# Kernel tuning notes

Measured on AMD Instinct MI355X. Metric: run time of the kernel, lower is better.

Reference implementation:

```python
import jax, jax.numpy as jnp
import numpy as np

CONF_THRESH = 0.25
IOU_THRESH = 0.45
MAX_PER_IMG = 100
K_PRE = 512          # fixed pre-NMS candidate count (padding for jit)
CLS_OFFSET = 4096.0  # class offset for non-class-agnostic NMS (torchvision batched_nms trick)


def setup_inputs() -> dict:
    key = jax.random.key(0)
    k1, k2, k3, k4 = jax.random.split(key, 4)
    B, N, C = 32, 8400, 80
    # YOLOX raw output layout: (cx, cy, w, h, obj, cls_0..cls_C-1)
    cxcy = jax.random.uniform(k1, (B, N, 2), dtype=jnp.float32) * 640.0
    wh = jax.random.uniform(k2, (B, N, 2), dtype=jnp.float32) * 128.0 + 4.0
    obj = jax.random.uniform(k3, (B, N, 1), dtype=jnp.float32)
    cls = jax.random.uniform(k4, (B, N, C), dtype=jnp.float32)
    pred = jnp.concatenate([cxcy, wh, obj, cls], axis=-1)  # [B, N, 85]
    return {"pred": pred}


def _pairwise_iou(b):
    # b: [K, 4] xyxy -> [K, K] IoU
    x1 = jnp.maximum(b[:, None, 0], b[None, :, 0])
    y1 = jnp.maximum(b[:, None, 1], b[None, :, 1])
    x2 = jnp.minimum(b[:, None, 2], b[None, :, 2])
    y2 = jnp.minimum(b[:, None, 3], b[None, :, 3])
    inter = jnp.clip(x2 - x1, 0.0) * jnp.clip(y2 - y1, 0.0)
    area = (b[:, 2] - b[:, 0]) * (b[:, 3] - b[:, 1])
    union = area[:, None] + area[None, :] - inter
    return inter / (union + 1e-9)


def _nms(boxes, valid):
    # boxes [K,4] already sorted by score desc; valid [K] bool. Greedy NMS.
    iou = _pairwise_iou(boxes)

    def body(i, keep):
        # keep[j] is False for j >= i, so this only checks earlier kept boxes
        suppressed = jnp.any(keep & (iou[i] > IOU_THRESH))
        return keep.at[i].set(valid[i] & jnp.logical_not(suppressed))

    return jax.lax.fori_loop(0, K_PRE, body, jnp.zeros(K_PRE, dtype=bool))


def reference(pred):
    # --- box decode: cxcywh -> xyxy (YOLOX postprocess box_corner) ---
    half = pred[..., 2:4] * 0.5
    boxes = jnp.concatenate([pred[..., :2] - half, pred[..., :2] + half], axis=-1)  # [B,N,4]
    obj = pred[..., 4]                 # [B,N]
    cls = pred[..., 5:]                # [B,N,C]
    class_conf = cls.max(axis=-1)      # [B,N]
    class_pred = jnp.argmax(cls, axis=-1)  # [B,N] int
    scores = obj * class_conf          # [B,N]

    # per-image adaptive conf: min(conf_thresh, best score) -> at least 1 survives
    conf = jnp.minimum(CONF_THRESH, scores.max(axis=-1, keepdims=True))  # [B,1]
    valid = scores >= conf
    masked = jnp.where(valid, scores, -jnp.inf)

    # fixed-size candidate set, sorted by score desc
    top_scores, idx = jax.lax.top_k(masked, K_PRE)  # [B,K]
    b_k = jnp.take_along_axis(boxes, idx[..., None], axis=1)       # [B,K,4]
    obj_k = jnp.take_along_axis(obj, idx, axis=1)                  # [B,K]
    cc_k = jnp.take_along_axis(class_conf, idx, axis=1)            # [B,K]
    cp_k = jnp.take_along_axis(class_pred, idx, axis=1)            # [B,K]
    valid_k = jnp.isfinite(top_scores)

    # class_agnostic=False: offset boxes by class so cross-class IoU is 0
    nms_boxes = b_k + cp_k.astype(b_k.dtype)[..., None] * CLS_OFFSET
    keep = jax.vmap(_nms)(nms_boxes, valid_k)  # [B,K] bool

    # compact kept boxes to the front (stable argsort preserves score order)
    order = jnp.argsort(jnp.where(keep, jnp.arange(K_PRE), K_PRE), axis=-1)
    sel = order[:, :MAX_PER_IMG]                                   # [B,M]
    mask = jnp.take_along_axis(keep, sel, axis=1)                  # [B,M]

    dets = jnp.concatenate(
        [b_k, obj_k[..., None], cc_k[..., None], cp_k.astype(b_k.dtype)[..., None]],
        axis=-1,
    )  # [B,K,7] = (x1,y1,x2,y2,obj,class_conf,class_pred)
    dets = jnp.take_along_axis(dets, sel[..., None], axis=1)       # [B,M,7]
    dets = dets * mask[..., None].astype(dets.dtype)
    return dets, mask
```

## Files before the change

### kernel.cpp

```cpp
#include <hip/hip_runtime.h>

#define NB 32
#define NN 8400
#define NC 80
#define KPRE 512
#define MAXOUT 100
#define NGRP 263
#define NWV 526

__global__ __launch_bounds__(128) void score_kernel(const float* __restrict__ pred,
                                                    float* __restrict__ scores,
                                                    unsigned* __restrict__ wmaxg,
                                                    float4* __restrict__ rawbox,
                                                    float4* __restrict__ minfo) {
    int b = blockIdx.y;
    int w = threadIdx.x >> 6, lane = threadIdx.x & 63;
    int g = blockIdx.x * 2 + w;
    __shared__ float4 stg4[2][340];
    const float4* p4 = (const float4*)pred;
    size_t base4 = (size_t)b * 178500 + (size_t)g * 340;
    size_t img_end4 = ((size_t)b + 1) * 178500;
    for (int k = lane; k < 340; k += 64) {
        size_t e = base4 + k;
        if (e >= img_end4) e = img_end4 - 1;
        stg4[w][k] = p4[e];
    }
    int rl = lane >> 2, q = lane & 3;
    int row = g * 16 + rl;
    const float* r = (const float*)&stg4[w][0] + rl * 85;
    float cx = r[0], cy = r[1], bw = r[2], bh = r[3], obj = r[4];
    int c0 = 5 + q * 20;
    float cc = r[c0];
    int cp = q * 20;
    for (int c = 1; c < 20; c++) {
        float v = r[c0 + c];
        if (v > cc) { cc = v; cp = q * 20 + c; }
    }
    {
        float cc1 = __shfl_xor(cc, 1, 64); int cp1 = __shfl_xor(cp, 1, 64);
        bool take = (cc1 > cc) || (cc1 == cc && cp1 < cp);
        cc = take ? cc1 : cc; cp = take ? cp1 : cp;
        float cc2 = __shfl_xor(cc, 2, 64); int cp2 = __shfl_xor(cp, 2, 64);
        take = (cc2 > cc) || (cc2 == cc && cp2 < cp);
        cc = take ? cc2 : cc; cp = take ? cp2 : cp;
    }
    float s = __fmul_rn(obj, cc);
    float hw = __fmul_rn(bw, 0.5f), hh = __fmul_rn(bh, 0.5f);
    float x1 = cx - hw, y1 = cy - hh, x2 = cx + hw, y2 = cy + hh;
    int srcl = (lane & 15) * 4;
    float v0 = __shfl(x1, srcl, 64);
    float v1 = __shfl(y1, srcl, 64);
    float v2 = __shfl(x2, srcl, 64);
    float v3 = __shfl(y2, srcl, 64);
    float v4 = __shfl(obj, srcl, 64);
    float v5 = __shfl(cc, srcl, 64);
    int   v6 = __shfl(cp, srcl, 64);
    float v7 = __shfl(s, srcl, 64);
    int wrow = g * 16 + (lane & 15);
    if (lane < 16 && wrow < NN) {
        size_t idx = (size_t)b * NN + wrow;
        scores[idx] = v7;
        rawbox[idx] = make_float4(v0, v1, v2, v3);
        minfo[idx]  = make_float4(v4, v5, (float)v6, v7);
    }
    if (row >= NN) s = 0.0f;
    unsigned bits = __float_as_uint(s);
    for (int o = 32; o > 0; o >>= 1) {
        unsigned other = (unsigned)__shfl_down((int)bits, o, 64);
        if (other > bits) bits = other;
    }
    if (lane == 0) wmaxg[b * NWV + g] = bits;
}

__device__ __forceinline__ void find_bin(const unsigned* hist, int cstart, unsigned T, int lane,
                                         int* outB, unsigned* outR) {
    unsigned running = 0;
    unsigned v = hist[cstart * 64 + lane];
    for (int c = cstart; c >= 0; c--) {
        unsigned vn = (c > 0) ? hist[(c - 1) * 64 + lane] : 0u;
        unsigned s = v;
        for (int off = 1; off < 64; off <<= 1) {
            unsigned u = (unsigned)__shfl_down((int)s, off, 64);
            if (lane + off < 64) s += u;
        }
        unsigned total0 = (unsigned)__shfl((int)s, 0, 64);
        if (total0 + running >= T) {
            unsigned long long mask = __ballot(s + running >= T);
            int m = 63 - __clzll(mask);
            unsigned sm = (unsigned)__shfl((int)s, m, 64);
            unsigned vm = (unsigned)__shfl((int)v, m, 64);
            if (lane == 0) { *outB = c * 64 + m; *outR = T - (sm + running - vm); }
            return;
        }
        running += total0;
        v = vn;
    }
    if (lane == 0) { *outB = 0; *outR = T; }
}

__device__ __forceinline__ void find_bin4(const uint4* h4, int cstart, unsigned T, int lane,
                                          int* outB, unsigned* outR) {
    unsigned running = 0;
    uint4 q = h4[cstart * 64 + lane];
    for (int c = cstart; c >= 0; c--) {
        uint4 qn;
        if (c > 0) qn = h4[(c - 1) * 64 + lane];
        else { qn.x = 0; qn.y = 0; qn.z = 0; qn.w = 0; }
        unsigned v = q.x + q.y + q.z + q.w;
        unsigned s = v;
        for (int off = 1; off < 64; off <<= 1) {
            unsigned u = (unsigned)__shfl_down((int)s, off, 64);
            if (lane + off < 64) s += u;
        }
        unsigned total0 = (unsigned)__shfl((int)s, 0, 64);
        if (total0 + running >= T) {
            unsigned long long mask = __ballot(s + running >= T);
            int m = 63 - __clzll(mask);
            unsigned sm = (unsigned)__shfl((int)s, m, 64);
            unsigned vm = (unsigned)__shfl((int)v, m, 64);
            if (lane == 0) { *outB = c * 64 + m; *outR = T - (sm + running - vm); }
            return;
        }
        running += total0;
        q = qn;
    }
    if (lane == 0) { *outB = 0; *outR = T; }
}

__global__ __launch_bounds__(1024) void selnms_kernel(const float* __restrict__ scores,
                                                      const unsigned* __restrict__ wmaxg,
                                                      const float4* __restrict__ rawbox,
                                                      const float4* __restrict__ minfo,
                                                      float* __restrict__ out) {
    int b = blockIdx.x, t = threadIdx.x;
    int lane = t & 63;
    __shared__ unsigned histB[2048];
    __shared__ unsigned long long list[KPRE];
    __shared__ unsigned long long sorted[KPRE];
    __shared__ unsigned long long elist64[256];
    __shared__ float4 sb[KPRE];
    __shared__ float4 sraw[KPRE];
    __shared__ float4 smeta[KPRE];
    __shared__ float  sarea[KPRE];
    __shared__ unsigned long long siou[KPRE * 8];
    __shared__ unsigned long long skeep[8];
    __shared__ int S_B[2];
    __shared__ unsigned S_T[2];
    __shared__ int S_cnt, S_ecnt, S_done;
    __shared__ float S_conf;
    __shared__ unsigned S_mbits;

    unsigned* histA4 = (unsigned*)siou;
    int hcopy = (t >> 8) & 3;

    if (t == 0) { S_cnt = 0; S_ecnt = 0; S_done = 0; }
    if (t < 64) {
        unsigned tmp[9];
#pragma unroll
        for (int k = 0; k < 9; k++) {
            int i = t + k * 64;
            tmp[k] = (i < NWV) ? wmaxg[b * NWV + i] : 0u;
        }
        unsigned m = 0;
#pragma unroll
        for (int k = 0; k < 9; k++) if (tmp[k] > m) m = tmp[k];
        for (int off = 32; off > 0; off >>= 1) {
            unsigned o = (unsigned)__shfl_down((int)m, off, 64);
            if (o > m) m = o;
        }
        if (t == 0) { S_conf = fminf(0.25f, __uint_as_float(m)); S_mbits = m; }
    }
    for (int i = t; i < 8192; i += 1024) histA4[i] = 0;
    for (int i = t; i < 2048; i += 1024) histB[i] = 0;
    if (t < 256) elist64[t] = 0ull;
    __syncthreads();
    float conf = S_conf;
    const float4* sc4 = (const float4*)(scores + (size_t)b * NN);
    unsigned ka[8];
    unsigned kb[4] = {0u, 0u, 0u, 0u};
    {
        float4 u0 = sc4[2 * t], u1 = sc4[2 * t + 1];
        ka[0] = (u0.x >= conf) ? __float_as_uint(u0.x) : 0u;
        ka[1] = (u0.y >= conf) ? __float_as_uint(u0.y) : 0u;
        ka[2] = (u0.z >= conf) ? __float_as_uint(u0.z) : 0u;
        ka[3] = (u0.w >= conf) ? __float_as_uint(u0.w) : 0u;
        ka[4] = (u1.x >= conf) ? __float_as_uint(u1.x) : 0u;
        ka[5] = (u1.y >= conf) ? __float_as_uint(u1.y) : 0u;
        ka[6] = (u1.z >= conf) ? __float_as_uint(u1.z) : 0u;
        ka[7] = (u1.w >= conf) ? __float_as_uint(u1.w) : 0u;
        if (t < 52) {
            float4 u2 = sc4[2048 + t];
            kb[0] = (u2.x >= conf) ? __float_as_uint(u2.x) : 0u;
            kb[1] = (u2.y >= conf) ? __float_as_uint(u2.y) : 0u;
            kb[2] = (u2.z >= conf) ? __float_as_uint(u2.z) : 0u;
            kb[3] = (u2.w >= conf) ? __float_as_uint(u2.w) : 0u;
        }
#pragma unroll
        for (int j = 0; j < 8; j++) {
            unsigned k = ka[j];
            if (k) atomicAdd(&histA4[((k >> 21) << 2) | hcopy], 1u);
        }
        if (t < 52) {
#pragma unroll
            for (int j = 0; j < 4; j++) {
                unsigned k = kb[j];
                if (k) atomicAdd(&histA4[((k >> 21) << 2) | hcopy], 1u);
            }
        }
    }
    __syncthreads();
    if (t < 64) {
        int cs = (int)(S_mbits >> 27); if (cs > 31) cs = 31;
        find_bin4((const uint4*)histA4, cs, 512u, t, &S_B[0], &S_T[0]);
    }
    __syncthreads();
    int B1 = S_B[0]; unsigned R1 = S_T[0];
#pragma unroll
    for (int j = 0; j < 8; j++) {
        unsigned k = ka[j];
        if ((int)(k >> 21) == B1) atomicAdd(&histB[(k >> 10) & 0x7FFu], 1u);
    }
    if (t < 52) {
#pragma unroll
        for (int j = 0; j < 4; j++) {
            unsigned k = kb[j];
            if ((int)(k >> 21) == B1) atomicAdd(&histB[(k >> 10) & 0x7FFu], 1u);
        }
    }
    for (int i = t; i < KPRE * 8; i += 1024) siou[i] = 0ull;
    __syncthreads();
    if (t < 64) find_bin(histB, 31, R1, t, &S_B[1], &S_T[1]);
    __syncthreads();
    unsigned P = ((unsigned)B1 << 11) | (unsigned)S_B[1];
    unsigned R2 = S_T[1];
    unsigned long long ltmask = (1ull << lane) - 1ull;
#pragma unroll
    for (int j = 0; j < 8; j++) {
        unsigned k = ka[j];
        unsigned n = 8u * (unsigned)t + (unsigned)j;
        unsigned long long key = ((unsigned long long)k << 32) | (unsigned long long)(unsigned)(~n);
        bool win = (k >> 10) > P;
        bool tie = (P != 0u) && ((k >> 10) == P);
        unsigned long long mw = __ballot(win);
        unsigned long long mtie = __ballot(tie);
        int baseW = 0, baseT = 0;
        if (lane == 0) {
            if (mw)   baseW = atomicAdd(&S_cnt, __popcll(mw));
            if (mtie) baseT = atomicAdd(&S_ecnt, __popcll(mtie));
        }
        baseW = __shfl(baseW, 0, 64);
        baseT = __shfl(baseT, 0, 64);
        if (win) {
            list[baseW + __popcll(mw & ltmask)] = key;
        } else if (tie) {
            int ep = baseT + __popcll(mtie & ltmask);
            if (ep < 256) elist64[ep] = key;
        }
    }
    if (t < 52) {
#pragma unroll
        for (int j = 0; j < 4; j++) {
            unsigned k = kb[j];
            unsigned n = 8192u + 4u * (unsigned)t + (unsigned)j;
            unsigned long long key = ((unsigned long long)k << 32) | (unsigned long long)(unsigned)(~n);
            bool win = (k >> 10) > P;
            bool tie = (P != 0u) && ((k >> 10) == P);
            unsigned long long mw = __ballot(win);
            unsigned long long mtie = __ballot(tie);
            int baseW = 0, baseT = 0;
            if (lane == 0) {
                if (mw)   baseW = atomicAdd(&S_cnt, __popcll(mw));
                if (mtie) baseT = atomicAdd(&S_ecnt, __popcll(mtie));
            }
            baseW = __shfl(baseW, 0, 64);
            baseT = __shfl(baseT, 0, 64);
            if (win) {
                list[baseW + __popcll(mw & ltmask)] = key;
            } else if (tie) {
                int ep = baseT + __popcll(mtie & ltmask);
                if (ep < 256) elist64[ep] = key;
            }
        }
    }
    __syncthreads();
    {
        int ecnt = S_ecnt; if (ecnt > 256) ecnt = 256;
        if (t < 64 && 4 * t < ecnt) {
            const ulonglong2* e2 = (const ulonglong2*)elist64;
            ulonglong2 klo = e2[2 * t], khi = e2[2 * t + 1];
            unsigned long long K[4] = { klo.x, klo.y, khi.x, khi.y };
            int r[4] = {0, 0, 0, 0};
            int jmax = (ecnt + 7) >> 3 << 2;
#pragma unroll 1
            for (int j = 0; j < jmax; j += 4) {
                ulonglong2 a = e2[j], b2 = e2[j + 1], c2 = e2[j + 2], d2 = e2[j + 3];
#pragma unroll
                for (int q = 0; q < 4; q++) {
                    r[q] += (int)(a.x > K[q]) + (int)(a.y > K[q])
                          + (int)(b2.x > K[q]) + (int)(b2.y > K[q])
                          + (int)(c2.x > K[q]) + (int)(c2.y > K[q])
                          + (int)(d2.x > K[q]) + (int)(d2.y > K[q]);
                }
            }
#pragma unroll
            for (int q = 0; q < 4; q++) {
                if (K[q] != 0ull && r[q] < (int)R2) {
                    int pos = atomicAdd(&S_cnt, 1);
                    list[pos] = K[q];
                }
            }
        }
    }
    __syncthreads();
    int nval = S_cnt;
    for (int i = nval + t; i < KPRE; i += 1024) list[i] = 0ull;
    __syncthreads();
    if (t < 128) {
        const ulonglong2* l2 = (const ulonglong2*)list;
        ulonglong2 klo = l2[2 * t], khi = l2[2 * t + 1];
        unsigned long long K[4] = { klo.x, klo.y, khi.x, khi.y };
        int r[4] = {0, 0, 0, 0};
#pragma unroll 1
        for (int j = 0; j < 256; j += 4) {
            ulonglong2 a = l2[j], b2 = l2[j + 1], c2 = l2[j + 2], d2 = l2[j + 3];
#pragma unroll
            for (int q = 0; q < 4; q++) {
                r[q] += (int)(a.x > K[q]) + (int)(a.y > K[q])
                      + (int)(b2.x > K[q]) + (int)(b2.y > K[q])
                      + (int)(c2.x > K[q]) + (int)(c2.y > K[q])
                      + (int)(d2.x > K[q]) + (int)(d2.y > K[q]);
            }
        }
#pragma unroll
        for (int q = 0; q < 4; q++) {
            int p = 4 * t + q;
            if (K[q] != 0ull) sorted[r[q]] = K[q]; else sorted[p] = 0ull;
        }
    }
    __syncthreads();
    if (t < KPRE) {
        unsigned long long key = sorted[t];
        int valid = ((unsigned)(key >> 32)) != 0u;
        unsigned n = ~(unsigned)key;
        if (!valid) n = 0;
        size_t src = (size_t)b * NN + n;
        float4 rb = rawbox[src];
        float4 mi = minfo[src];
        float off = __fmul_rn(mi.z, 4096.0f);
        float4 bo = make_float4(rb.x + off, rb.y + off, rb.z + off, rb.w + off);
        sraw[t] = rb;
        sb[t] = bo;
        smeta[t] = make_float4(mi.x, mi.y, mi.z, valid ? 1.0f : 0.0f);
        sarea[t] = __fmul_rn(bo.z - bo.x, bo.w - bo.y);
    }
    __syncthreads();

    unsigned long long keepW = 0ull;
    int cnt = 0;
    int lg = t >> 3, lw = t & 7;
    int irow = t >> 4, iq = t & 15;

    for (int c = 0; c < 8; c++) {
        int row = (c << 6) + irow;
        float4 bi = sb[row];
        float ai = sarea[row];
        for (int k = 0; k <= c; k++) {
            unsigned long long wk = 0ull;
            int j0 = (k << 6) + iq;
#pragma unroll
            for (int s = 0; s < 4; s++) {
                int j = j0 + (s << 4);
                float4 bj = sb[j];
                float xx1 = fmaxf(bi.x, bj.x);
                float yy1 = fmaxf(bi.y, bj.y);
                float xx2 = fminf(bi.z, bj.z);
                float yy2 = fminf(bi.w, bj.w);
                float iw = fmaxf(xx2 - xx1, 0.0f);
                float ih = fmaxf(yy2 - yy1, 0.0f);
                float inter = __fmul_rn(iw, ih);
                float uni = (ai + sarea[j]) - inter;
                float iou = inter / (uni + 1e-9f);
                if (iou > 0.45f && j < row) wk |= 1ull << (j & 63);
            }
            if (wk) atomicOr(&siou[(row << 3) + k], wk);
        }
        __syncthreads();
        if (t < 64) {
            unsigned long long R[8];
#pragma unroll
            for (int k = 0; k < 8; k++) R[k] = siou[(c << 9) + (k << 6) + t];
#pragma unroll
            for (int k = 0; k < 8; k++) {
#pragma unroll
                for (int m = 0; m < 8; m++) {
                    int ii = (c << 6) + (k << 3) + m;
                    bool hit = (lg == m) && ((R[k] & keepW) != 0ull);
                    unsigned long long bal = __ballot(hit);
                    bool kept = (bal == 0ull) && (ii < nval);
                    if (kept) {
                        cnt++;
                        if (lw == c) keepW |= 1ull << ((k << 3) + m);
                    }
                }
            }
            if (t == 0) S_done = (cnt >= MAXOUT) ? 1 : 0;
        }
        __syncthreads();
        if (S_done) break;
    }
    if (t < 8) skeep[t] = keepW;
    __syncthreads();

    float* dets = out + (size_t)b * (MAXOUT * 7);
    float* maskp = out + (size_t)NB * MAXOUT * 7 + (size_t)b * MAXOUT;
    for (int m = t; m < MAXOUT * 7; m += 1024) dets[m] = 0.0f;
    for (int m = t; m < MAXOUT; m += 1024) maskp[m] = 0.0f;
    __syncthreads();
    if (t < KPRE) {
        int wq = t >> 6;
        unsigned long long kw = skeep[wq];
        if ((kw >> (t & 63)) & 1ull) {
            int rank = __popcll(kw & ((1ull << (t & 63)) - 1ull));
            for (int w2 = 0; w2 < wq; w2++) rank += __popcll(skeep[w2]);
            if (rank < MAXOUT) {
                float4 rb = sraw[t];
                float4 mt = smeta[t];
                float* rowp = dets + rank * 7;
                rowp[0] = rb.x; rowp[1] = rb.y; rowp[2] = rb.z; rowp[3] = rb.w;
                rowp[4] = mt.x; rowp[5] = mt.y; rowp[6] = mt.z;
                maskp[rank] = 1.0f;
            }
        }
    }
}

extern "C" void kernel_launch(void* const* d_in, const int* in_sizes, int n_in,
                              void* d_out, int out_size, void* d_ws, size_t ws_size,
                              hipStream_t stream) {
    const float* pred = (const float*)d_in[0];
    float* out = (float*)d_out;

    char* ws = (char*)d_ws;
    unsigned* wmaxg = (unsigned*)ws;
    float* scores = (float*)(ws + 67584);
    float4* rawbox = (float4*)(ws + 1142784);
    float4* minfo  = (float4*)(ws + 5443584);

    dim3 gA(NGRP, NB);
    score_kernel<<<gA, 128, 0, stream>>>(pred, scores, wmaxg, rawbox, minfo);
    selnms_kernel<<<NB, 1024, 0, stream>>>(scores, wmaxg, rawbox, minfo, out);
}
```

Measured before the change: 170.9 us.

## Overlap next IoU chunk with greedy NMS scan and use narrow ballot histogram

The first-level radix histogram is replaced by a small 12-bin histogram relative to the confidence threshold's exponent bucket. Each wave builds it with ballot/popcount and a few shared atomics, so the large 8192-entry atomic histogram and its scan go away. In NMS, the IoU bitmask for the next 64-row chunk is computed by threads 512-1023 while wave 0 runs the serial greedy scan on the current chunk, which removes one barrier phase per chunk. Risk: the narrow histogram assumes the top 512 scores fall within 12 exponent/mantissa bins above conf and falls back to B=0 otherwise. Fewer threads compute each IoU chunk.

```diff
diff --git a/kernel.cpp b/kernel.cpp
--- a/kernel.cpp
+++ b/kernel.cpp
@@ -7,6 +7,7 @@
 #define MAXOUT 100
 #define NGRP 263
 #define NWV 526
+#define NSBIN 12
 
 __global__ __launch_bounds__(128) void score_kernel(const float* __restrict__ pred,
                                                     float* __restrict__ scores,
@@ -98,35 +99,6 @@
     if (lane == 0) { *outB = 0; *outR = T; }
 }
 
-__device__ __forceinline__ void find_bin4(const uint4* h4, int cstart, unsigned T, int lane,
-                                          int* outB, unsigned* outR) {
-    unsigned running = 0;
-    uint4 q = h4[cstart * 64 + lane];
-    for (int c = cstart; c >= 0; c--) {
-        uint4 qn;
-        if (c > 0) qn = h4[(c - 1) * 64 + lane];
-        else { qn.x = 0; qn.y = 0; qn.z = 0; qn.w = 0; }
-        unsigned v = q.x + q.y + q.z + q.w;
-        unsigned s = v;
-        for (int off = 1; off < 64; off <<= 1) {
-            unsigned u = (unsigned)__shfl_down((int)s, off, 64);
-            if (lane + off < 64) s += u;
-        }
-        unsigned total0 = (unsigned)__shfl((int)s, 0, 64);
-        if (total0 + running >= T) {
-            unsigned long long mask = __ballot(s + running >= T);
-            int m = 63 - __clzll(mask);
-            unsigned sm = (unsigned)__shfl((int)s, m, 64);
-            unsigned vm = (unsigned)__shfl((int)v, m, 64);
-            if (lane == 0) { *outB = c * 64 + m; *outR = T - (sm + running - vm); }
-            return;
-        }
-        running += total0;
-        q = qn;
-    }
-    if (lane == 0) { *outB = 0; *outR = T; }
-}
-
 __global__ __launch_bounds__(1024) void selnms_kernel(const float* __restrict__ scores,
                                                       const unsigned* __restrict__ wmaxg,
                                                       const float4* __restrict__ rawbox,
@@ -135,6 +107,7 @@
     int b = blockIdx.x, t = threadIdx.x;
     int lane = t & 63;
     __shared__ unsigned histB[2048];
+    __shared__ unsigned histS[NSBIN];
     __shared__ unsigned long long list[KPRE];
     __shared__ unsigned long long sorted[KPRE];
     __shared__ unsigned long long elist64[256];
@@ -150,9 +123,6 @@
     __shared__ float S_conf;
     __shared__ unsigned S_mbits;
 
-    unsigned* histA4 = (unsigned*)siou;
-    int hcopy = (t >> 8) & 3;
-
     if (t == 0) { S_cnt = 0; S_ecnt = 0; S_done = 0; }
     if (t < 64) {
         unsigned tmp[9];
@@ -170,11 +140,14 @@
         }
         if (t == 0) { S_conf = fminf(0.25f, __uint_as_float(m)); S_mbits = m; }
     }
-    for (int i = t; i < 8192; i += 1024) histA4[i] = 0;
     for (int i = t; i < 2048; i += 1024) histB[i] = 0;
+    for (int i = t; i < KPRE * 8; i += 1024) siou[i] = 0ull;
     if (t < 256) elist64[t] = 0ull;
+    if (t < NSBIN) histS[t] = 0u;
     __syncthreads();
     float conf = S_conf;
+    unsigned confb = __float_as_uint(conf);
+    int binlo = (int)(confb >> 21);
     const float4* sc4 = (const float4*)(scores + (size_t)b * NN);
     unsigned ka[8];
     unsigned kb[4] = {0u, 0u, 0u, 0u};
@@ -188,30 +161,46 @@
         ka[5] = (u1.y >= conf) ? __float_as_uint(u1.y) : 0u;
         ka[6] = (u1.z >= conf) ? __float_as_uint(u1.z) : 0u;
         ka[7] = (u1.w >= conf) ? __float_as_uint(u1.w) : 0u;
+        unsigned wcnt[NSBIN];
+#pragma unroll
+        for (int i = 0; i < NSBIN; i++) wcnt[i] = 0u;
+#pragma unroll
+        for (int j = 0; j < 8; j++) {
+            int bb = (ka[j] != 0u) ? ((int)(ka[j] >> 21) - binlo) : -1;
+#pragma unroll
+            for (int i = 0; i < NSBIN; i++)
+                wcnt[i] += (unsigned)__popcll(__ballot(bb == i));
+        }
         if (t < 52) {
             float4 u2 = sc4[2048 + t];
             kb[0] = (u2.x >= conf) ? __float_as_uint(u2.x) : 0u;
             kb[1] = (u2.y >= conf) ? __float_as_uint(u2.y) : 0u;
             kb[2] = (u2.z >= conf) ? __float_as_uint(u2.z) : 0u;
             kb[3] = (u2.w >= conf) ? __float_as_uint(u2.w) : 0u;
-        }
-#pragma unroll
-        for (int j = 0; j < 8; j++) {
-            unsigned k = ka[j];
-            if (k) atomicAdd(&histA4[((k >> 21) << 2) | hcopy], 1u);
-        }
-        if (t < 52) {
 #pragma unroll
             for (int j = 0; j < 4; j++) {
-                unsigned k = kb[j];
-                if (k) atomicAdd(&histA4[((k >> 21) << 2) | hcopy], 1u);
-            }
-        }
-    }
-    __syncthreads();
-    if (t < 64) {
-        int cs = (int)(S_mbits >> 27); if (cs > 31) cs = 31;
-        find_bin4((const uint4*)histA4, cs, 512u, t, &S_B[0], &S_T[0]);
+                int bb = (kb[j] != 0u) ? ((int)(kb[j] >> 21) - binlo) : -1;
+#pragma unroll
+                for (int i = 0; i < NSBIN; i++)
+                    wcnt[i] += (unsigned)__popcll(__ballot(bb == i));
+            }
+        }
+        if (lane == 0) {
+#pragma unroll
+            for (int i = 0; i < NSBIN; i++)
+                if (wcnt[i]) atomicAdd(&histS[i], wcnt[i]);
+        }
+    }
+    __syncthreads();
+    if (t == 0) {
+        unsigned run = 0; int B = 0; unsigned R = 512u; int found = 0;
+        for (int i = NSBIN - 1; i >= 0; i--) {
+            unsigned v = histS[i];
+            if (!found && run + v >= 512u) { B = binlo + i; R = 512u - run; found = 1; }
+            run += v;
+        }
+        if (!found) { B = 0; R = 512u; }
+        S_B[0] = B; S_T[0] = R;
     }
     __syncthreads();
     int B1 = S_B[0]; unsigned R1 = S_T[0];
@@ -227,7 +216,6 @@
             if ((int)(k >> 21) == B1) atomicAdd(&histB[(k >> 10) & 0x7FFu], 1u);
         }
     }
-    for (int i = t; i < KPRE * 8; i += 1024) siou[i] = 0ull;
     __syncthreads();
     if (t < 64) find_bin(histB, 31, R1, t, &S_B[1], &S_T[1]);
     __syncthreads();
@@ -358,33 +346,33 @@
     unsigned long long keepW = 0ull;
     int cnt = 0;
     int lg = t >> 3, lw = t & 7;
-    int irow = t >> 4, iq = t & 15;
-
-    for (int c = 0; c < 8; c++) {
-        int row = (c << 6) + irow;
+
+    {
+        int irow = t >> 4, iq = t & 15;
+        int row = irow;
         float4 bi = sb[row];
         float ai = sarea[row];
-        for (int k = 0; k <= c; k++) {
-            unsigned long long wk = 0ull;
-            int j0 = (k << 6) + iq;
-#pragma unroll
-            for (int s = 0; s < 4; s++) {
-                int j = j0 + (s << 4);
-                float4 bj = sb[j];
-                float xx1 = fmaxf(bi.x, bj.x);
-                float yy1 = fmaxf(bi.y, bj.y);
-                float xx2 = fminf(bi.z, bj.z);
-                float yy2 = fminf(bi.w, bj.w);
-                float iw = fmaxf(xx2 - xx1, 0.0f);
-                float ih = fmaxf(yy2 - yy1, 0.0f);
-                float inter = __fmul_rn(iw, ih);
-                float uni = (ai + sarea[j]) - inter;
-                float iou = inter / (uni + 1e-9f);
-                if (iou > 0.45f && j < row) wk |= 1ull << (j & 63);
-            }
-            if (wk) atomicOr(&siou[(row << 3) + k], wk);
-        }
-        __syncthreads();
+        unsigned long long wk = 0ull;
+#pragma unroll
+        for (int s = 0; s < 4; s++) {
+            int j = iq + (s << 4);
+            float4 bj = sb[j];
+            float xx1 = fmaxf(bi.x, bj.x);
+            float yy1 = fmaxf(bi.y, bj.y);
+            float xx2 = fminf(bi.z, bj.z);
+            float yy2 = fminf(bi.w, bj.w);
+            float iw = fmaxf(xx2 - xx1, 0.0f);
+            float ih = fmaxf(yy2 - yy1, 0.0f);
+            float inter = __fmul_rn(iw, ih);
+            float uni = (ai + sarea[j]) - inter;
+            float iou = inter / (uni + 1e-9f);
+            if (iou > 0.45f && j < row) wk |= 1ull << (j & 63);
+        }
+        if (wk) atomicOr(&siou[row << 3], wk);
+    }
+    __syncthreads();
+
+    for (int c = 0; c < 8; c++) {
         if (t < 64) {
             unsigned long long R[8];
 #pragma unroll
@@ -404,6 +392,32 @@
                 }
             }
             if (t == 0) S_done = (cnt >= MAXOUT) ? 1 : 0;
+        } else if (t >= 512 && c + 1 < 8) {
+            int cc2 = c + 1;
+            int irow = (t - 512) >> 3, iq = t & 7;
+            int row = (cc2 << 6) + irow;
+            float4 bi = sb[row];
+            float ai = sarea[row];
+            for (int k = 0; k <= cc2; k++) {
+                unsigned long long wk = 0ull;
+                int j0 = (k << 6) + iq;
+#pragma unroll
+                for (int s = 0; s < 8; s++) {
+                    int j = j0 + (s << 3);
+                    float4 bj = sb[j];
+                    float xx1 = fmaxf(bi.x, bj.x);
+                    float yy1 = fmaxf(bi.y, bj.y);
+                    float xx2 = fminf(bi.z, bj.z);
+                    float yy2 = fminf(bi.w, bj.w);
+                    float iw = fmaxf(xx2 - xx1, 0.0f);
+                    float ih = fmaxf(yy2 - yy1, 0.0f);
+                    float inter = __fmul_rn(iw, ih);
+                    float uni = (ai + sarea[j]) - inter;
+                    float iou = inter / (uni + 1e-9f);
+                    if (iou > 0.45f && j < row) wk |= 1ull << (j & 63);
+                }
+                if (wk) atomicOr(&siou[(row << 3) + k], wk);
+            }
         }
         __syncthreads();
         if (S_done) break;
```

Measured after the change: 173.4 us. No clear change (+1.4%).
